# Kernel optimization log

Measured on AMD Instinct MI355X. Metric: run time of the kernel, lower is better.

The kernel has to match this reference:

```python
import jax, jax.numpy as jnp
import numpy as np
from jax.ops import segment_sum, segment_max

N_NODES, SEQ, D, V = 2048, 64, 256, 32000
NH, DH = 8, 32      # transformer heads, head dim
GH = 4              # GAT heads (concat=False -> mean over heads)
E = 32768
NEG_INF = -1e9


def _pe(max_len, d):
    pos = np.arange(max_len)[:, None].astype(np.float32)
    div = np.exp(np.arange(0, d, 2).astype(np.float32) * (-np.log(10000.0) / d))
    pe = np.zeros((max_len, d), np.float32)
    pe[:, 0::2] = np.sin(pos * div)
    pe[:, 1::2] = np.cos(pos * div)
    return jnp.asarray(pe)


def _ln(x, g, b, eps=1e-5):
    m = x.mean(-1, keepdims=True)
    v = jnp.var(x, axis=-1, keepdims=True)
    return (x - m) / jnp.sqrt(v + eps) * g + b


def _encoder(x, Wqkv, bqkv, Wo, bo, ln1g, ln1b, ln2g, ln2b, W1, b1, W2, b2):
    # nn.TransformerEncoder, post-norm, relu, dropout off (eval)
    for l in range(2):
        qkv = x @ Wqkv[l] + bqkv[l]
        q, k, v = jnp.split(qkv, 3, -1)
        hds = lambda t: t.reshape(N_NODES, SEQ, NH, DH).transpose(0, 2, 1, 3)
        q, k, v = hds(q), hds(k), hds(v)
        att = jax.nn.softmax(jnp.einsum('bhqd,bhkd->bhqk', q, k) / np.sqrt(DH).astype(np.float32), -1)
        o = jnp.einsum('bhqk,bhkd->bhqd', att, v).transpose(0, 2, 1, 3).reshape(N_NODES, SEQ, D)
        x = _ln(x + o @ Wo[l] + bo[l], ln1g[l], ln1b[l])
        ff = jax.nn.relu(x @ W1[l] + b1[l]) @ W2[l] + b2[l]
        x = _ln(x + ff, ln2g[l], ln2b[l])
    return x


def _gat(xt, W, b, asrc, adst, src, dst, emask):
    # PyG GATConv(heads=4, concat=False): self-loops added, LeakyReLU(0.2),
    # softmax over incoming edges per destination, mean over heads, + bias.
    x = (xt @ W).reshape(N_NODES, GH, D)              # [N,GH,D]
    a_s = jnp.sum(x * asrc, -1)                        # [N,GH]
    a_d = jnp.sum(x * adst, -1)
    e = jax.nn.leaky_relu(a_s[src] + a_d[dst], 0.2)    # [E,GH]
    e = jnp.where(emask[:, None], e, NEG_INF)
    e_self = jax.nn.leaky_relu(a_s + a_d, 0.2)         # [N,GH] self loops
    m = jnp.maximum(segment_max(e, dst, num_segments=N_NODES), e_self)
    w = jnp.where(emask[:, None], jnp.exp(e - m[dst]), 0.0)
    w_self = jnp.exp(e_self - m)
    denom = segment_sum(w, dst, num_segments=N_NODES) + w_self
    num = segment_sum(w[:, :, None] * x[src], dst, num_segments=N_NODES) + w_self[:, :, None] * x
    return (num / denom[:, :, None]).mean(1) + b


def setup_inputs():
    key = jax.random.key(0)
    ks = iter(jax.random.split(key, 40))
    g = lambda shape, s=0.02: jax.random.normal(next(ks), shape, jnp.float32) * s
    return dict(
        tok_emb=g((V, D)),
        enc_Wqkv=g((2, D, 3 * D)), enc_bqkv=jnp.zeros((2, 3 * D)),
        enc_Wo=g((2, D, D)), enc_bo=jnp.zeros((2, D)),
        enc_ln1_g=jnp.ones((2, D)), enc_ln1_b=jnp.zeros((2, D)),
        enc_ln2_g=jnp.ones((2, D)), enc_ln2_b=jnp.zeros((2, D)),
        enc_W1=g((2, D, D)), enc_b1=jnp.zeros((2, D)),
        enc_W2=g((2, D, D)), enc_b2=jnp.zeros((2, D)),
        type_emb=g((10, D)),
        msg_W=g((3, D, D)), msg_b=jnp.zeros((3, D)),
        gat_W=g((4, D, GH * D)), gat_b=jnp.zeros((4, D)),
        gat_asrc=g((4, GH, D)), gat_adst=g((4, GH, D)),
        sp_W1=g((D, 512)), sp_b1=jnp.zeros((512,)),
        sp_W2=g((512, D)), sp_b2=jnp.zeros((D,)),
        log_c=jnp.zeros((1,)),
        rule_token_seqs=jax.random.randint(next(ks), (N_NODES, SEQ), 0, V),
        rule_types=jax.random.randint(next(ks), (N_NODES,), 0, 10),
        edge_index=jax.random.randint(next(ks), (2, E), 0, N_NODES),
        edge_type=jax.random.randint(next(ks), (E,), 0, 3),
    )


def reference(tok_emb, enc_Wqkv, enc_bqkv, enc_Wo, enc_bo, enc_ln1_g, enc_ln1_b,
              enc_ln2_g, enc_ln2_b, enc_W1, enc_b1, enc_W2, enc_b2, type_emb,
              msg_W, msg_b, gat_W, gat_b, gat_asrc, gat_adst,
              sp_W1, sp_b1, sp_W2, sp_b2, log_c,
              rule_token_seqs, rule_types, edge_index, edge_type):
    # logic encoder
    x = tok_emb[rule_token_seqs] * np.sqrt(D).astype(np.float32) + _pe(SEQ, D)[None]
    x = _encoder(x, enc_Wqkv, enc_bqkv, enc_Wo, enc_bo, enc_ln1_g, enc_ln1_b,
                 enc_ln2_g, enc_ln2_b, enc_W1, enc_b1, enc_W2, enc_b2)
    h = x.mean(1) + type_emb[rule_types]                 # node_features [N,D]
    # logical GNN: per-relation linear + GATConv, summed, residual, relu
    src, dst = edge_index[0], edge_index[1]
    for l in range(4):
        h_new = 0.0
        for r in range(3):
            th = h @ msg_W[r] + msg_b[r]
            h_new = h_new + _gat(th, gat_W[l], gat_b[l], gat_asrc[l], gat_adst[l],
                                 src, dst, edge_type == r)
        h = jax.nn.relu(h + h_new)
    pos = jax.nn.relu(h @ sp_W1 + sp_b1) @ sp_W2 + sp_b2
    tang = jnp.tanh(pos) * 2.0
    st = tang * jnp.sqrt(jnp.exp(log_c))                 # scaled tangent [N,D]
    # Lorentz exp_map0 of v = [0, st]: ||v||_L = ||st||
    r = jnp.maximum(jnp.linalg.norm(st, axis=-1, keepdims=True), 1e-8)
    return jnp.concatenate([jnp.cosh(r), jnp.sinh(r) / r * st], -1)  # [N, D+1]
```

## Files before the change

### kernel.cpp

```cpp
#include <hip/hip_runtime.h>
#include <hip/hip_bf16.h>

#define NN 2048
#define SEQL 64
#define DIM 256
#define NHEAD 8
#define EDGES 32768
#define CROWS (NN * SEQL)
#define CHUNKS 2
#define CN (NN / CHUNKS)
#define CRC (CROWS / CHUNKS)

typedef __attribute__((ext_vector_type(8))) short short8;
typedef __attribute__((ext_vector_type(4))) float f32x4;
typedef __attribute__((ext_vector_type(4))) unsigned short us4;
typedef unsigned short ushort_t;

__device__ __forceinline__ float us2f(unsigned short u) {
    union { unsigned int i; float f; } x; x.i = ((unsigned int)u) << 16; return x.f;
}
__device__ __forceinline__ unsigned short f2us(float f) {
    union { float f; unsigned int i; } u; u.f = f;
    unsigned int r = u.i + 0x7fffu + ((u.i >> 16) & 1u);
    return (unsigned short)(r >> 16);
}
__device__ __forceinline__ float lrelu02(float v) { return v < 0.f ? 0.2f * v : v; }

__device__ __forceinline__ void gload_lds16(const void* g, void* l) {
    __builtin_amdgcn_global_load_lds(
        (const __attribute__((address_space(1))) unsigned int*)g,
        (__attribute__((address_space(3))) unsigned int*)l, 16, 0, 0);
}

__global__ void sniff_kernel(const unsigned int* __restrict__ w, int* __restrict__ flag) {
    __shared__ int cnt;
    if (threadIdx.x == 0) cnt = 0;
    __syncthreads();
    unsigned int v = w[(size_t)threadIdx.x * 509];
    unsigned int e_lo = (v >> 7) & 0xffu;
    if (e_lo >= 0x6eu && e_lo <= 0x7fu) atomicAdd(&cnt, 1);
    __syncthreads();
    if (threadIdx.x == 0) *flag = (cnt > 128) ? 1 : 0;
}

#define NE 33
struct ConvArgs {
    const void* src[NE];
    unsigned int soff[NE];
    unsigned int off[NE + 1];
    unsigned int nel[NE];
    unsigned short ncol[NE];
    unsigned char klog2[NE];
};

__global__ void convert_kernel(ConvArgs a, const int* __restrict__ flag,
                               ushort_t* __restrict__ dst, unsigned int total) {
    const int bf = *flag;
    for (unsigned int i = blockIdx.x * 256 + threadIdx.x; i < total; i += gridDim.x * 256) {
        int e = 0;
        while (a.off[e + 1] <= i) ++e;
        unsigned int j = i - a.off[e];
        ushort_t v = 0;
        if (j < a.nel[e]) {
            unsigned int sidx;
            if (a.klog2[e]) {
                unsigned int K = 1u << a.klog2[e];
                unsigned int k = j & (K - 1), n = j >> a.klog2[e];
                sidx = k * (unsigned int)a.ncol[e] + n;
            } else sidx = j;
            sidx += a.soff[e];
            if (bf) v = ((const ushort_t*)a.src[e])[sidx];
            else    v = f2us(((const float*)a.src[e])[sidx]);
        }
        dst[i] = v;
    }
}

template <int K, bool RELU, bool OUT_BF16>
__global__ __launch_bounds__(256) void gemm_bt(
    const ushort_t* __restrict__ A, const ushort_t* __restrict__ BT,
    const ushort_t* __restrict__ bias, void* __restrict__ C,
    int N, int lda, size_t a_off_z, size_t c_off_z)
{
    __shared__ __align__(16) short smem[16384];

    const int tid  = threadIdx.x;
    const int lane = tid & 63;
    const int wave = tid >> 6;
    const int wr = wave >> 1, wc = wave & 1;

    const int gx = gridDim.x, gy = gridDim.y;
    const int nwg = gx * gy;
    const int lin = blockIdx.y * gx + blockIdx.x;
    const int q8 = nwg >> 3;
    const int sid = (lin & 7) * q8 + (lin >> 3);
    const int mb = sid / gy;
    const int nb = sid - mb * gy;
    const size_t mbase = (size_t)mb * 128;
    const size_t nbase = (size_t)nb * 128;

    A += (size_t)blockIdx.z * a_off_z;
    const size_t czoff = (size_t)blockIdx.z * c_off_z;

    f32x4 acc[4][4];
    const f32x4 fzero = {0.f, 0.f, 0.f, 0.f};
#pragma unroll
    for (int i = 0; i < 4; ++i)
#pragma unroll
        for (int j = 0; j < 4; ++j) acc[i][j] = fzero;

    const int srow = tid >> 2;
    const int ksw0 = (((tid & 3) ^ ((srow >> 1) & 3)) * 8);
    const int rl = lane & 15;
    const int kfs = (((lane >> 4) ^ ((rl >> 1) & 3)) * 8);

    constexpr int nk = K >> 5;
    auto stage = [&](int buf, int k0) {
        short* lA = smem + buf * 4096 + wave * 512;
        short* lB = smem + 8192 + buf * 4096 + wave * 512;
        gload_lds16(A  + (mbase + srow)      * (size_t)lda + k0 + ksw0, lA);
        gload_lds16(A  + (mbase + srow + 64) * (size_t)lda + k0 + ksw0, lA + 2048);
        gload_lds16(BT + (nbase + srow)      * (size_t)K   + k0 + ksw0, lB);
        gload_lds16(BT + (nbase + srow + 64) * (size_t)K   + k0 + ksw0, lB + 2048);
    };

    stage(0, 0);
    if (nk > 1) stage(1, 32);
#pragma unroll
    for (int t = 0; t < nk; ++t) {
        const int cur = t & 1;
        if (t + 1 < nk) { asm volatile("s_waitcnt vmcnt(4)" ::: "memory"); }
        else            { asm volatile("s_waitcnt vmcnt(0)" ::: "memory"); }
        __builtin_amdgcn_s_barrier();
        __builtin_amdgcn_sched_barrier(0);

        short8 af[4], bfr[4];
#pragma unroll
        for (int m = 0; m < 4; ++m)
            af[m]  = *(const short8*)&smem[cur * 4096 + (wr * 64 + m * 16 + rl) * 32 + kfs];
#pragma unroll
        for (int n = 0; n < 4; ++n)
            bfr[n] = *(const short8*)&smem[8192 + cur * 4096 + (wc * 64 + n * 16 + rl) * 32 + kfs];
        asm volatile("s_waitcnt lgkmcnt(0)" ::: "memory");
        __builtin_amdgcn_sched_barrier(0);
#pragma unroll
        for (int m = 0; m < 4; ++m)
#pragma unroll
            for (int n = 0; n < 4; ++n)
                acc[m][n] = __builtin_amdgcn_mfma_f32_16x16x32_bf16(af[m], bfr[n], acc[m][n], 0, 0, 0);
        __builtin_amdgcn_s_barrier();
        __builtin_amdgcn_sched_barrier(0);
        if (t + 2 < nk) stage(cur, (t + 2) * 32);
    }

    const int rq = (lane >> 4) * 4;
    if (OUT_BF16) {
#pragma unroll
        for (int m = 0; m < 4; ++m)
#pragma unroll
            for (int n = 0; n < 4; ++n) {
                int lcol = wc * 64 + n * 16 + rl;
                float bv = bias ? us2f(bias[nbase + lcol]) : 0.f;
                int chunk = lcol >> 3;
#pragma unroll
                for (int q = 0; q < 4; ++q) {
                    int row = wr * 64 + m * 16 + rq + q;
                    float v = acc[m][n][q] + bv;
                    if (RELU) v = fmaxf(v, 0.f);
                    smem[row * 128 + (((chunk ^ (row & 7)) << 3) | (lcol & 7))] = (short)f2us(v);
                }
            }
        asm volatile("s_waitcnt lgkmcnt(0)" ::: "memory");
        __builtin_amdgcn_s_barrier();
        __builtin_amdgcn_sched_barrier(0);
#pragma unroll
        for (int j = 0; j < 8; ++j) {
            int hw = tid * 8 + j * 2048;
            int row = hw >> 7;
            int ch  = tid & 15;
            short8 v = *(const short8*)&smem[row * 128 + ((ch ^ (row & 7)) << 3)];
            *(short8*)((ushort_t*)C + czoff + (mbase + row) * (size_t)N + nbase + ch * 8) = v;
        }
    } else {
#pragma unroll
        for (int m = 0; m < 4; ++m)
#pragma unroll
            for (int n = 0; n < 4; ++n) {
                size_t gcol = nbase + wc * 64 + n * 16 + rl;
                float bv = bias ? us2f(bias[gcol]) : 0.f;
#pragma unroll
                for (int q = 0; q < 4; ++q) {
                    size_t grow = mbase + wr * 64 + m * 16 + rq + q;
                    float v = acc[m][n][q] + bv;
                    if (RELU) v = fmaxf(v, 0.f);
                    ((float*)C)[czoff + grow * N + gcol] = v;
                }
            }
    }
}

template <int K>
__global__ __launch_bounds__(512) void gemm_ln(
    const ushort_t* __restrict__ A, int lda, const ushort_t* __restrict__ BT,
    const ushort_t* __restrict__ bias, ushort_t* __restrict__ X,
    const ushort_t* __restrict__ gg, const ushort_t* __restrict__ bb)
{
    __shared__ __align__(16) short a_lds[2][128][32];
    __shared__ __align__(16) short b_lds[2][256][32];
    __shared__ float st_part[128][8];
    __shared__ float st_fin[128][2];

    const int tid  = threadIdx.x;
    const int lane = tid & 63;
    const int wave = tid >> 6;
    const int wr = wave >> 2, wc = wave & 3;
    const size_t mbase = (size_t)blockIdx.x * 128;

    f32x4 acc[4][4];
    const f32x4 fzero = {0.f, 0.f, 0.f, 0.f};
#pragma unroll
    for (int i = 0; i < 4; ++i)
#pragma unroll
        for (int j = 0; j < 4; ++j) acc[i][j] = fzero;

    const int srow = tid >> 2;
    const int ksw0 = (((tid & 3) ^ ((srow >> 1) & 3)) * 8);
    const int rl = lane & 15;
    const int g  = lane >> 4;
    const int kfs = ((g ^ ((rl >> 1) & 3)) * 8);

    constexpr int nk = K >> 5;
    auto stage = [&](int buf, int k0) {
        gload_lds16(A  + (mbase + srow) * (size_t)lda + k0 + ksw0,
                    &a_lds[buf][0][0] + wave * 512);
        gload_lds16(BT + (size_t)srow         * K + k0 + ksw0,
                    &b_lds[buf][0][0] + wave * 512);
        gload_lds16(BT + (size_t)(srow + 128) * K + k0 + ksw0,
                    &b_lds[buf][0][0] + wave * 512 + 4096);
    };

    stage(0, 0);
    if (nk > 1) stage(1, 32);
#pragma unroll
    for (int t = 0; t < nk; ++t) {
        const int cur = t & 1;
        if (t + 1 < nk) { asm volatile("s_waitcnt vmcnt(3)" ::: "memory"); }
        else            { asm volatile("s_waitcnt vmcnt(0)" ::: "memory"); }
        __builtin_amdgcn_s_barrier();
        __builtin_amdgcn_sched_barrier(0);

        short8 af[4], bfr[4];
#pragma unroll
        for (int m = 0; m < 4; ++m) af[m]  = *(const short8*)&a_lds[cur][wr * 64 + m * 16 + rl][kfs];
#pragma unroll
        for (int n = 0; n < 4; ++n) bfr[n] = *(const short8*)&b_lds[cur][wc * 64 + n * 16 + rl][kfs];
        asm volatile("s_waitcnt lgkmcnt(0)" ::: "memory");
        __builtin_amdgcn_sched_barrier(0);
#pragma unroll
        for (int m = 0; m < 4; ++m)
#pragma unroll
            for (int n = 0; n < 4; ++n)
                acc[m][n] = __builtin_amdgcn_mfma_f32_16x16x32_bf16(af[m], bfr[n], acc[m][n], 0, 0, 0);
        __builtin_amdgcn_s_barrier();
        __builtin_amdgcn_sched_barrier(0);
        if (t + 2 < nk) stage(cur, (t + 2) * 32);
    }

#pragma unroll
    for (int m = 0; m < 4; ++m)
#pragma unroll
        for (int n = 0; n < 4; ++n) {
            int gcol = wc * 64 + n * 16 + rl;
            float bv = us2f(bias[gcol]);
#pragma unroll
            for (int r = 0; r < 4; ++r) {
                size_t grow = mbase + wr * 64 + m * 16 + g * 4 + r;
                acc[m][n][r] += bv + us2f(X[grow * 256 + gcol]);
            }
        }
#pragma unroll
    for (int m = 0; m < 4; ++m)
#pragma unroll
        for (int r = 0; r < 4; ++r) {
            float ps = 0.f, pq = 0.f;
#pragma unroll
            for (int n = 0; n < 4; ++n) { float v = acc[m][n][r]; ps += v; pq += v * v; }
#pragma unroll
            for (int off = 1; off < 16; off <<= 1) { ps += __shfl_xor(ps, off); pq += __shfl_xor(pq, off); }
            if (rl == 0) {
                int row = wr * 64 + m * 16 + g * 4 + r;
                st_part[row][wc] = ps;
                st_part[row][4 + wc] = pq;
            }
        }
    __syncthreads();
    if (tid < 128) {
        float s = st_part[tid][0] + st_part[tid][1] + st_part[tid][2] + st_part[tid][3];
        float q = st_part[tid][4] + st_part[tid][5] + st_part[tid][6] + st_part[tid][7];
        float mean = s * (1.f / 256.f);
        float var = q * (1.f / 256.f) - mean * mean;
        st_fin[tid][0] = mean;
        st_fin[tid][1] = rsqrtf(var + 1e-5f);
    }
    __syncthreads();
#pragma unroll
    for (int m = 0; m < 4; ++m)
#pragma unroll
        for (int n = 0; n < 4; ++n) {
            int gcol = wc * 64 + n * 16 + rl;
            float gv = us2f(gg[gcol]), bv = us2f(bb[gcol]);
#pragma unroll
            for (int r = 0; r < 4; ++r) {
                int row = wr * 64 + m * 16 + g * 4 + r;
                float out = (acc[m][n][r] - st_fin[row][0]) * st_fin[row][1] * gv + bv;
                X[(mbase + row) * 256 + gcol] = f2us(out);
            }
        }
}

__global__ __launch_bounds__(256) void ffn_ln(
    ushort_t* __restrict__ X,
    const ushort_t* __restrict__ W1T, const ushort_t* __restrict__ b1,
    const ushort_t* __restrict__ W2T, const ushort_t* __restrict__ b2,
    const ushort_t* __restrict__ gg, const ushort_t* __restrict__ bb)
{
    __shared__ __align__(16) short a_lds[2][64][32];
    __shared__ __align__(16) short b_lds[2][256][32];
    __shared__ __align__(16) short T[64 * 256];
    __shared__ float st_part[64][8];
    __shared__ float st_fin[64][2];

    const int tid  = threadIdx.x;
    const int lane = tid & 63;
    const int wc   = tid >> 6;
    const size_t mbase = (size_t)blockIdx.x * 64;
    const int rl = lane & 15;
    const int g  = lane >> 4;
    const int kfs = ((g ^ ((rl >> 1) & 3)) * 8);

    const int arow = tid >> 2;
    const int ksw0 = (((tid & 3) ^ ((arow >> 1) & 3)) * 8);

    f32x4 acc[4][4];
    const f32x4 fzero = {0.f, 0.f, 0.f, 0.f};
#pragma unroll
    for (int i = 0; i < 4; ++i)
#pragma unroll
        for (int j = 0; j < 4; ++j) acc[i][j] = fzero;

    auto stage1 = [&](int buf, int k0) {
        gload_lds16(X + (mbase + arow) * (size_t)256 + k0 + ksw0,
                    &a_lds[buf][0][0] + wc * 512);
#pragma unroll
        for (int p = 0; p < 4; ++p)
            gload_lds16(W1T + (size_t)(arow + p * 64) * 256 + k0 + ksw0,
                        &b_lds[buf][0][0] + p * 2048 + wc * 512);
    };
    auto stage2 = [&](int buf, int k0) {
#pragma unroll
        for (int p = 0; p < 4; ++p)
            gload_lds16(W2T + (size_t)(arow + p * 64) * 256 + k0 + ksw0,
                        &b_lds[buf][0][0] + p * 2048 + wc * 512);
    };

    stage1(0, 0);
    stage1(1, 32);
#pragma unroll
    for (int t = 0; t < 8; ++t) {
        const int cur = t & 1;
        if (t + 1 < 8) { asm volatile("s_waitcnt vmcnt(5)" ::: "memory"); }
        else           { asm volatile("s_waitcnt vmcnt(0)" ::: "memory"); }
        __builtin_amdgcn_s_barrier();
        __builtin_amdgcn_sched_barrier(0);

        short8 af[4], bfr[4];
#pragma unroll
        for (int m = 0; m < 4; ++m) af[m]  = *(const short8*)&a_lds[cur][m * 16 + rl][kfs];
#pragma unroll
        for (int n = 0; n < 4; ++n) bfr[n] = *(const short8*)&b_lds[cur][wc * 64 + n * 16 + rl][kfs];
        asm volatile("s_waitcnt lgkmcnt(0)" ::: "memory");
        __builtin_amdgcn_sched_barrier(0);
#pragma unroll
        for (int m = 0; m < 4; ++m)
#pragma unroll
            for (int n = 0; n < 4; ++n)
                acc[m][n] = __builtin_amdgcn_mfma_f32_16x16x32_bf16(af[m], bfr[n], acc[m][n], 0, 0, 0);
        __builtin_amdgcn_s_barrier();
        __builtin_amdgcn_sched_barrier(0);
        if (t + 2 < 8) stage1(cur, (t + 2) * 32);
    }

    stage2(0, 0);
    stage2(1, 32);

#pragma unroll
    for (int m = 0; m < 4; ++m)
#pragma unroll
        for (int n = 0; n < 4; ++n) {
            int lcol = wc * 64 + n * 16 + rl;
            float bv = us2f(b1[lcol]);
            int chunk = lcol >> 3;
#pragma unroll
            for (int q = 0; q < 4; ++q) {
                int row = m * 16 + g * 4 + q;
                float v = fmaxf(acc[m][n][q] + bv, 0.f);
                T[row * 256 + (((chunk ^ (row & 7)) << 3) | (lcol & 7))] = (short)f2us(v);
            }
            acc[m][n] = fzero;
        }
    asm volatile("s_waitcnt lgkmcnt(0)" ::: "memory");
    __builtin_amdgcn_s_barrier();
    __builtin_amdgcn_sched_barrier(0);

#pragma unroll
    for (int t = 0; t < 8; ++t) {
        const int cur = t & 1;
        if (t + 1 < 8) { asm volatile("s_waitcnt vmcnt(4)" ::: "memory"); }
        else           { asm volatile("s_waitcnt vmcnt(0)" ::: "memory"); }
        __builtin_amdgcn_s_barrier();
        __builtin_amdgcn_sched_barrier(0);

        short8 af[4], bfr[4];
#pragma unroll
        for (int m = 0; m < 4; ++m) {
            int row = m * 16 + rl;
            af[m] = *(const short8*)&T[row * 256 + (((t * 4 + g) ^ (row & 7)) << 3)];
        }
#pragma unroll
        for (int n = 0; n < 4; ++n) bfr[n] = *(const short8*)&b_lds[cur][wc * 64 + n * 16 + rl][kfs];
        asm volatile("s_waitcnt lgkmcnt(0)" ::: "memory");
        __builtin_amdgcn_sched_barrier(0);
#pragma unroll
        for (int m = 0; m < 4; ++m)
#pragma unroll
            for (int n = 0; n < 4; ++n)
                acc[m][n] = __builtin_amdgcn_mfma_f32_16x16x32_bf16(af[m], bfr[n], acc[m][n], 0, 0, 0);
        __builtin_amdgcn_s_barrier();
        __builtin_amdgcn_sched_barrier(0);
        if (t + 2 < 8) stage2(cur, (t + 2) * 32);
    }

#pragma unroll
    for (int m = 0; m < 4; ++m)
#pragma unroll
        for (int n = 0; n < 4; ++n) {
            int gcol = wc * 64 + n * 16 + rl;
            float bv = us2f(b2[gcol]);
#pragma unroll
            for (int r = 0; r < 4; ++r) {
                size_t grow = mbase + m * 16 + g * 4 + r;
                acc[m][n][r] += bv + us2f(X[grow * 256 + gcol]);
            }
        }
#pragma unroll
    for (int m = 0; m < 4; ++m)
#pragma unroll
        for (int r = 0; r < 4; ++r) {
            float ps = 0.f, pq = 0.f;
#pragma unroll
            for (int n = 0; n < 4; ++n) { float v = acc[m][n][r]; ps += v; pq += v * v; }
#pragma unroll
            for (int off = 1; off < 16; off <<= 1) { ps += __shfl_xor(ps, off); pq += __shfl_xor(pq, off); }
            if (rl == 0) {
                int row = m * 16 + g * 4 + r;
                st_part[row][wc] = ps;
                st_part[row][4 + wc] = pq;
            }
        }
    __syncthreads();
    if (tid < 64) {
        float s = st_part[tid][0] + st_part[tid][1] + st_part[tid][2] + st_part[tid][3];
        float q = st_part[tid][4] + st_part[tid][5] + st_part[tid][6] + st_part[tid][7];
        float mean = s * (1.f / 256.f);
        float var = q * (1.f / 256.f) - mean * mean;
        st_fin[tid][0] = mean;
        st_fin[tid][1] = rsqrtf(var + 1e-5f);
    }
    __syncthreads();
#pragma unroll
    for (int m = 0; m < 4; ++m)
#pragma unroll
        for (int n = 0; n < 4; ++n) {
            int gcol = wc * 64 + n * 16 + rl;
            float gv = us2f(gg[gcol]), bv = us2f(bb[gcol]);
#pragma unroll
            for (int r = 0; r < 4; ++r) {
                int row = m * 16 + g * 4 + r;
                float out = (acc[m][n][r] - st_fin[row][0]) * st_fin[row][1] * gv + bv;
                X[(mbase + row) * 256 + gcol] = f2us(out);
            }
        }
}

__global__ __launch_bounds__(128) void attn_mfma(ushort_t* __restrict__ qkv) {
    __shared__ ushort_t smem[2][6912];
    const int w = threadIdx.x >> 6, lane = threadIdx.x & 63;
    const int h = blockIdx.y * 2 + w;
    const int rl = lane & 15, g = lane >> 4;
    const size_t rowbase = (size_t)blockIdx.x * 64;
    ushort_t* vt = smem[w];
    ushort_t* pl = smem[w] + 2304;

    const ushort_t* vp = qkv + (rowbase + lane) * 768 + 512 + h * 32;
#pragma unroll
    for (int i = 0; i < 4; ++i) {
        union { short8 v; ushort_t s[8]; } u;
        u.v = *(const short8*)(vp + i * 8);
#pragma unroll
        for (int j = 0; j < 8; ++j) vt[(i * 8 + j) * 72 + lane] = u.s[j];
    }

    short8 kf[4], qf[4];
#pragma unroll
    for (int t = 0; t < 4; ++t) {
        kf[t] = *(const short8*)(qkv + (rowbase + t * 16 + rl) * 768 + 256 + h * 32 + g * 8);
        qf[t] = *(const short8*)(qkv + (rowbase + t * 16 + rl) * 768 +       h * 32 + g * 8);
    }

    f32x4 s[4][4];
    const f32x4 fzero = {0.f, 0.f, 0.f, 0.f};
#pragma unroll
    for (int kt = 0; kt < 4; ++kt)
#pragma unroll
        for (int qt = 0; qt < 4; ++qt) s[kt][qt] = fzero;
#pragma unroll
    for (int kt = 0; kt < 4; ++kt)
#pragma unroll
        for (int qt = 0; qt < 4; ++qt)
            s[kt][qt] = __builtin_amdgcn_mfma_f32_16x16x32_bf16(kf[kt], qf[qt], s[kt][qt], 0, 0, 0);

    const float sc = 0.17677669529663687f;
    float inv[4];
#pragma unroll
    for (int qt = 0; qt < 4; ++qt) {
        float m = -1e30f;
#pragma unroll
        for (int kt = 0; kt < 4; ++kt)
#pragma unroll
            for (int r = 0; r < 4; ++r) { s[kt][qt][r] *= sc; m = fmaxf(m, s[kt][qt][r]); }
        m = fmaxf(m, __shfl_xor(m, 16));
        m = fmaxf(m, __shfl_xor(m, 32));
        float sum = 0.f;
#pragma unroll
        for (int kt = 0; kt < 4; ++kt)
#pragma unroll
            for (int r = 0; r < 4; ++r) { float e = __expf(s[kt][qt][r] - m); s[kt][qt][r] = e; sum += e; }
        sum += __shfl_xor(sum, 16);
        sum += __shfl_xor(sum, 32);
        inv[qt] = 1.f / sum;
    }

#pragma unroll
    for (int qt = 0; qt < 4; ++qt)
#pragma unroll
        for (int kt = 0; kt < 4; ++kt) {
            us4 pk;
#pragma unroll
            for (int r = 0; r < 4; ++r) pk[r] = f2us(s[kt][qt][r] * inv[qt]);
            *(us4*)&pl[(qt * 16 + rl) * 72 + kt * 16 + g * 4] = pk;
        }
    asm volatile("s_waitcnt lgkmcnt(0)" ::: "memory");
    __builtin_amdgcn_sched_barrier(0);

    f32x4 o[2][4];
#pragma unroll
    for (int dt = 0; dt < 2; ++dt)
#pragma unroll
        for (int qt = 0; qt < 4; ++qt) o[dt][qt] = fzero;
#pragma unroll
    for (int ks = 0; ks < 2; ++ks) {
        short8 va[2];
#pragma unroll
        for (int dt = 0; dt < 2; ++dt)
            va[dt] = *(const short8*)&vt[(dt * 16 + rl) * 72 + ks * 32 + g * 8];
#pragma unroll
        for (int qt = 0; qt < 4; ++qt) {
            short8 pb = *(const short8*)&pl[(qt * 16 + rl) * 72 + ks * 32 + g * 8];
#pragma unroll
            for (int dt = 0; dt < 2; ++dt)
                o[dt][qt] = __builtin_amdgcn_mfma_f32_16x16x32_bf16(va[dt], pb, o[dt][qt], 0, 0, 0);
        }
    }

#pragma unroll
    for (int dt = 0; dt < 2; ++dt)
#pragma unroll
        for (int qt = 0; qt < 4; ++qt) {
            us4 ov;
#pragma unroll
            for (int r = 0; r < 4; ++r) ov[r] = f2us(o[dt][qt][r]);
            *(us4*)&pl[(qt * 16 + rl) * 40 + dt * 16 + g * 4] = ov;
        }
    asm volatile("s_waitcnt lgkmcnt(0)" ::: "memory");
    __builtin_amdgcn_sched_barrier(0);
    ushort_t* op = qkv + (rowbase + lane) * 768 + h * 32;
#pragma unroll
    for (int t = 0; t < 4; ++t)
        *(short8*)(op + t * 8) = *(const short8*)&pl[lane * 40 + t * 8];
}

__global__ void pe_kernel(float* __restrict__ pe) {
    int s = blockIdx.x, d = threadIdx.x;
    int i = d >> 1;
    float freq = __expf((float)(2 * i) * (-9.210340371976184f / 256.f));
    float ang = (float)s * freq;
    pe[s * DIM + d] = (d & 1) ? cosf(ang) : sinf(ang);
}

__global__ __launch_bounds__(256) void embed_kernel(const void* __restrict__ tok_emb,
                                                    const int* __restrict__ flag,
                                                    const int* __restrict__ tokens,
                                                    const float* __restrict__ pe,
                                                    ushort_t* __restrict__ X) {
    int grow = blockIdx.x * 4 + (threadIdx.x >> 6);
    int t = threadIdx.x & 63;
    int tok = tokens[grow];
    int s = grow & 63;
    int d0 = t * 4;
    size_t idx = (size_t)tok * DIM + d0;
    f32x4 pv = *(const f32x4*)&pe[s * DIM + d0];
    us4 out;
    if (*flag) {
        us4 tv = *(const us4*)((const ushort_t*)tok_emb + idx);
#pragma unroll
        for (int j = 0; j < 4; ++j) out[j] = f2us(us2f(tv[j]) * 16.f + pv[j]);
    } else {
        f32x4 tv = *(const f32x4*)((const float*)tok_emb + idx);
#pragma unroll
        for (int j = 0; j < 4; ++j) out[j] = f2us(tv[j] * 16.f + pv[j]);
    }
    *(us4*)&X[(size_t)grow * DIM + d0] = out;
}

__global__ void mean_kernel(const ushort_t* __restrict__ Xc,
                            const ushort_t* __restrict__ type_emb,
                            const int* __restrict__ rtypes,
                            float* __restrict__ h, ushort_t* __restrict__ hb) {
    int n = blockIdx.x, d = threadIdx.x;
    float acc = 0.f;
    for (int s = 0; s < 64; ++s) acc += us2f(Xc[((size_t)n * 64 + s) * DIM + d]);
    float val = acc * (1.f / 64.f) + us2f(type_emb[(size_t)rtypes[n] * DIM + d]);
    h[(size_t)n * DIM + d] = val;
    hb[(size_t)n * DIM + d] = f2us(val);
}

__global__ void hist_kernel(const int* __restrict__ ei, int* __restrict__ counts) {
    int e = blockIdx.x * 256 + threadIdx.x;
    if (e < EDGES) atomicAdd(&counts[ei[EDGES + e]], 1);
}
__global__ __launch_bounds__(256) void scan_kernel(const int* __restrict__ counts,
                                                   int* __restrict__ indptr,
                                                   int* __restrict__ cursor) {
    __shared__ int part[256];
    int t = threadIdx.x;
    int local[8]; int s = 0;
#pragma unroll
    for (int i = 0; i < 8; ++i) { local[i] = s; s += counts[t * 8 + i]; }
    part[t] = s;
    __syncthreads();
    for (int d = 1; d < 256; d <<= 1) {
        int val = (t >= d) ? part[t - d] : 0;
        __syncthreads();
        part[t] += val;
        __syncthreads();
    }
    int base = part[t] - s;
#pragma unroll
    for (int i = 0; i < 8; ++i) { int v = base + local[i]; indptr[t * 8 + i] = v; cursor[t * 8 + i] = v; }
    if (t == 255) indptr[NN] = part[255];
}
__global__ void scatter_kernel(const int* __restrict__ ei, const int* __restrict__ et,
                               int* __restrict__ cursor, int* __restrict__ col_src,
                               int* __restrict__ col_type) {
    int e = blockIdx.x * 256 + threadIdx.x;
    if (e < EDGES) {
        int d = ei[EDGES + e];
        int pp = atomicAdd(&cursor[d], 1);
        col_src[pp] = ei[e];
        col_type[pp] = et[e];
    }
}

__global__ __launch_bounds__(256) void asad_kernel(const ushort_t* __restrict__ xg,
                                                   const ushort_t* __restrict__ asrc,
                                                   const ushort_t* __restrict__ adst,
                                                   float* __restrict__ a_s, float* __restrict__ a_d,
                                                   int l) {
    int n = blockIdx.x, r = blockIdx.y, g = threadIdx.x >> 6, lane = threadIdx.x & 63;
    const ushort_t* xp = xg + ((size_t)r * NN + n) * 1024 + g * 256 + lane * 4;
    const ushort_t* sp = asrc + ((size_t)l * 4 + g) * 256 + lane * 4;
    const ushort_t* dp = adst + ((size_t)l * 4 + g) * 256 + lane * 4;
    us4 xv = *(const us4*)xp;
    float ss = 0.f, dd = 0.f;
#pragma unroll
    for (int j = 0; j < 4; ++j) { float x = us2f(xv[j]); ss += x * us2f(sp[j]); dd += x * us2f(dp[j]); }
#pragma unroll
    for (int off = 32; off > 0; off >>= 1) { ss += __shfl_xor(ss, off); dd += __shfl_xor(dd, off); }
    if (lane == 0) {
        a_s[((size_t)r * NN + n) * 4 + g] = ss;
        a_d[((size_t)r * NN + n) * 4 + g] = dd;
    }
}

__global__ __launch_bounds__(256) void edge_kernel(const ushort_t* __restrict__ xg,
                                                   const float* __restrict__ a_s,
                                                   const float* __restrict__ a_d,
                                                   const int* __restrict__ indptr,
                                                   const int* __restrict__ col_src,
                                                   const int* __restrict__ col_type,
                                                   const ushort_t* __restrict__ gat_b,
                                                   float* __restrict__ hnew3, int l) {
    __shared__ float outs[4][256];
    int n = blockIdx.x, r = blockIdx.y, g = threadIdx.x >> 6, lane = threadIdx.x & 63;
    int beg = indptr[n], end = indptr[n + 1];
    const size_t rb = (size_t)r * NN;
    float adn = a_d[(rb + n) * 4 + g];
    float eself = lrelu02(a_s[(rb + n) * 4 + g] + adn);
    float m = eself;
    for (int e = beg; e < end; ++e) {
        if (col_type[e] == r) {
            float v = lrelu02(a_s[(rb + col_src[e]) * 4 + g] + adn);
            m = fmaxf(m, v);
        }
    }
    float wself = __expf(eself - m);
    float denom = wself;
    us4 xn = *(const us4*)(xg + (rb + n) * 1024 + g * 256 + lane * 4);
    float num[4];
#pragma unroll
    for (int j = 0; j < 4; ++j) num[j] = wself * us2f(xn[j]);
    for (int e = beg; e < end; ++e) {
        if (col_type[e] == r) {
            int src = col_src[e];
            float v = lrelu02(a_s[(rb + src) * 4 + g] + adn);
            float w = __expf(v - m);
            denom += w;
            us4 xs = *(const us4*)(xg + (rb + src) * 1024 + g * 256 + lane * 4);
#pragma unroll
            for (int j = 0; j < 4; ++j) num[j] += w * us2f(xs[j]);
        }
    }
    float invd = 1.f / denom;
#pragma unroll
    for (int j = 0; j < 4; ++j) outs[g][lane * 4 + j] = num[j] * invd;
    __syncthreads();
    int d = threadIdx.x;
    float hv = 0.25f * (outs[0][d] + outs[1][d] + outs[2][d] + outs[3][d]) + us2f(gat_b[l * 256 + d]);
    hnew3[(rb + n) * 256 + d] = hv;
}

__global__ void update_h_kernel(float* __restrict__ h, const float* __restrict__ hnew3,
                                ushort_t* __restrict__ hb) {
    size_t i = (size_t)blockIdx.x * 256 + threadIdx.x;
    float v = fmaxf(h[i] + hnew3[i] + hnew3[(size_t)NN * 256 + i] + hnew3[(size_t)2 * NN * 256 + i], 0.f);
    h[i] = v;
    hb[i] = f2us(v);
}

__global__ __launch_bounds__(64) void final_kernel(const float* __restrict__ pos,
                                                   const ushort_t* __restrict__ log_c,
                                                   const int* __restrict__ flag,
                                                   void* __restrict__ out) {
    int n = blockIdx.x, lane = threadIdx.x;
    int bf = *flag;
    float scv = sqrtf(__expf(us2f(log_c[0])));
    f32x4 pv = *(const f32x4*)&pos[(size_t)n * 256 + lane * 4];
    float st[4]; float sq = 0.f;
#pragma unroll
    for (int j = 0; j < 4; ++j) { float t = tanhf(pv[j]) * 2.f * scv; st[j] = t; sq += t * t; }
#pragma unroll
    for (int off = 32; off > 0; off >>= 1) sq += __shfl_xor(sq, off);
    float rr = fmaxf(sqrtf(sq), 1e-8f);
    float sf = sinhf(rr) / rr;
    if (bf) {
        ushort_t* o = (ushort_t*)out;
        if (lane == 0) o[(size_t)n * 257] = f2us(coshf(rr));
#pragma unroll
        for (int j = 0; j < 4; ++j) o[(size_t)n * 257 + 1 + lane * 4 + j] = f2us(sf * st[j]);
    } else {
        float* o = (float*)out;
        if (lane == 0) o[(size_t)n * 257] = coshf(rr);
#pragma unroll
        for (int j = 0; j < 4; ++j) o[(size_t)n * 257 + 1 + lane * 4 + j] = sf * st[j];
    }
}

extern "C" void kernel_launch(void* const* d_in, const int* in_sizes, int n_in,
                              void* d_out, int out_size, void* d_ws, size_t ws_size,
                              hipStream_t stream) {
    const int* tokens = (const int*)d_in[25];
    const int* rtypes = (const int*)d_in[26];
    const int* eidx   = (const int*)d_in[27];
    const int* etype  = (const int*)d_in[28];

    char* base = (char*)d_ws;
    size_t pos = 0;
    auto alloc = [&](size_t b) -> char* {
        char* r = base + pos; pos = (pos + b + 255) & ~(size_t)255; return r;
    };

    int* flag = (int*)alloc(256);

    ConvArgs ca;
    int ne = 0; unsigned int off = 0;
    auto add = [&](const void* src, unsigned int soff, unsigned int elems,
                   int klog2, int ncol) -> unsigned int {
        ca.src[ne] = src; ca.soff[ne] = soff; ca.off[ne] = off;
        ca.nel[ne] = elems; ca.klog2[ne] = (unsigned char)klog2;
        ca.ncol[ne] = (unsigned short)ncol;
        unsigned int r = off; off += (elems + 7) & ~7u; ++ne; return r;
    };
    unsigned int oWqkv = add(d_in[1], 0, 196608, 8, 768);
                         add(d_in[1], 196608, 196608, 8, 768);
    unsigned int obqkv = add(d_in[2], 0, 1536, 0, 0);
    unsigned int oWo   = add(d_in[3], 0, 65536, 8, 256);
                         add(d_in[3], 65536, 65536, 8, 256);
    unsigned int obo   = add(d_in[4], 0, 512, 0, 0);
    unsigned int oln1g = add(d_in[5], 0, 512, 0, 0);
    unsigned int oln1b = add(d_in[6], 0, 512, 0, 0);
    unsigned int oln2g = add(d_in[7], 0, 512, 0, 0);
    unsigned int oln2b = add(d_in[8], 0, 512, 0, 0);
    unsigned int oW1   = add(d_in[9], 0, 65536, 8, 256);
                         add(d_in[9], 65536, 65536, 8, 256);
    unsigned int ob1   = add(d_in[10], 0, 512, 0, 0);
    unsigned int oW2   = add(d_in[11], 0, 65536, 8, 256);
                         add(d_in[11], 65536, 65536, 8, 256);
    unsigned int ob2   = add(d_in[12], 0, 512, 0, 0);
    unsigned int otype = add(d_in[13], 0, 2560, 0, 0);
    unsigned int omsgW = add(d_in[14], 0, 65536, 8, 256);
                         add(d_in[14], 65536, 65536, 8, 256);
                         add(d_in[14], 131072, 65536, 8, 256);
    unsigned int omsgb = add(d_in[15], 0, 768, 0, 0);
    unsigned int ogatW = add(d_in[16], 0, 262144, 8, 1024);
                         add(d_in[16], 262144, 262144, 8, 1024);
                         add(d_in[16], 524288, 262144, 8, 1024);
                         add(d_in[16], 786432, 262144, 8, 1024);
    unsigned int ogatb = add(d_in[17], 0, 1024, 0, 0);
    unsigned int oasrc = add(d_in[18], 0, 4096, 0, 0);
    unsigned int oadst = add(d_in[19], 0, 4096, 0, 0);
    unsigned int ospW1 = add(d_in[20], 0, 131072, 8, 512);
    unsigned int ospb1 = add(d_in[21], 0, 512, 0, 0);
    unsigned int ospW2 = add(d_in[22], 0, 131072, 9, 256);
    unsigned int ospb2 = add(d_in[23], 0, 256, 0, 0);
    unsigned int ologc = add(d_in[24], 0, 1, 0, 0);
    ca.off[ne] = off;
    unsigned int wtotal = off;

    ushort_t* wtb   = (ushort_t*)alloc((size_t)wtotal * 2);
    float*    pe    = (float*)   alloc((size_t)SEQL * DIM * 4);
    float*    h     = (float*)   alloc((size_t)NN * DIM * 4);
    ushort_t* hb    = (ushort_t*)alloc((size_t)NN * DIM * 2);
    float*    a_s   = (float*)   alloc((size_t)3 * NN * 4 * 4);
    float*    a_d   = (float*)   alloc((size_t)3 * NN * 4 * 4);
    int*      counts = (int*)    alloc((size_t)NN * 4);
    int*      indptr = (int*)    alloc((size_t)(NN + 1) * 4);
    int*      cursor = (int*)    alloc((size_t)NN * 4);
    int*      col_src  = (int*)  alloc((size_t)EDGES * 4);
    int*      col_type = (int*)  alloc((size_t)EDGES * 4);

    ushort_t* Xc  = (ushort_t*)alloc((size_t)CROWS * DIM * 2);
    size_t spos0 = pos;
    ushort_t* QKV = (ushort_t*)alloc((size_t)CRC * 768 * 2);
    pos = spos0;
    ushort_t* th    = (ushort_t*)alloc((size_t)NN * 768 * 2);
    ushort_t* xg    = (ushort_t*)alloc((size_t)3 * NN * 1024 * 2);
    float*    hnew3 = (float*)   alloc((size_t)3 * NN * DIM * 4);
    ushort_t* thead = (ushort_t*)alloc((size_t)NN * 512 * 2);
    float*    posb  = (float*)   alloc((size_t)NN * DIM * 4);

    const ushort_t* WqkvT = wtb + oWqkv;
    const ushort_t* bqkv  = wtb + obqkv;
    const ushort_t* WoT   = wtb + oWo;
    const ushort_t* bo    = wtb + obo;
    const ushort_t* ln1g  = wtb + oln1g;
    const ushort_t* ln1b  = wtb + oln1b;
    const ushort_t* ln2g  = wtb + oln2g;
    const ushort_t* ln2b  = wtb + oln2b;
    const ushort_t* W1T   = wtb + oW1;
    const ushort_t* b1    = wtb + ob1;
    const ushort_t* W2T   = wtb + oW2;
    const ushort_t* b2    = wtb + ob2;
    const ushort_t* type_emb = wtb + otype;
    const ushort_t* msgWT = wtb + omsgW;
    const ushort_t* msg_b = wtb + omsgb;
    const ushort_t* gatWT = wtb + ogatW;
    const ushort_t* gat_b = wtb + ogatb;
    const ushort_t* gasrc = wtb + oasrc;
    const ushort_t* gadst = wtb + oadst;
    const ushort_t* spW1T = wtb + ospW1;
    const ushort_t* spb1  = wtb + ospb1;
    const ushort_t* spW2T = wtb + ospW2;
    const ushort_t* spb2  = wtb + ospb2;
    const ushort_t* log_c = wtb + ologc;

    sniff_kernel<<<1, 256, 0, stream>>>((const unsigned int*)d_in[1], flag);
    convert_kernel<<<2048, 256, 0, stream>>>(ca, flag, wtb, wtotal);

    pe_kernel<<<SEQL, DIM, 0, stream>>>(pe);
    hipMemsetAsync(counts, 0, NN * 4, stream);
    hist_kernel<<<EDGES / 256, 256, 0, stream>>>(eidx, counts);
    scan_kernel<<<1, 256, 0, stream>>>(counts, indptr, cursor);
    scatter_kernel<<<EDGES / 256, 256, 0, stream>>>(eidx, etype, cursor, col_src, col_type);

    embed_kernel<<<CROWS / 4, 256, 0, stream>>>(d_in[0], flag, tokens, pe, Xc);
    for (int c = 0; c < CHUNKS; ++c) {
        ushort_t* Xcc = Xc + (size_t)c * CRC * DIM;
        for (int l = 0; l < 2; ++l) {
            gemm_bt<256, false, true><<<dim3(CRC / 128, 6), 256, 0, stream>>>(
                Xcc, WqkvT + (size_t)l * 196608, bqkv + l * 768, QKV, 768, DIM, 0, 0);
            attn_mfma<<<dim3(CN, 4), 128, 0, stream>>>(QKV);
            gemm_ln<256><<<CRC / 128, 512, 0, stream>>>(
                QKV, 768, WoT + (size_t)l * 65536, bo + l * DIM, Xcc, ln1g + l * DIM, ln1b + l * DIM);
            ffn_ln<<<CRC / 64, 256, 0, stream>>>(
                Xcc, W1T + (size_t)l * 65536, b1 + l * DIM, W2T + (size_t)l * 65536, b2 + l * DIM,
                ln2g + l * DIM, ln2b + l * DIM);
        }
    }
    mean_kernel<<<NN, DIM, 0, stream>>>(Xc, type_emb, rtypes, h, hb);

    for (int l = 0; l < 4; ++l) {
        gemm_bt<256, false, true><<<dim3(NN / 128, 6), 256, 0, stream>>>(
            hb, msgWT, msg_b, th, 768, DIM, 0, 0);
        gemm_bt<256, false, true><<<dim3(NN / 128, 8, 3), 256, 0, stream>>>(
            th, gatWT + (size_t)l * 262144, nullptr, xg, 1024, 768,
            (size_t)256, (size_t)NN * 1024);
        asad_kernel<<<dim3(NN, 3), 256, 0, stream>>>(xg, gasrc, gadst, a_s, a_d, l);
        edge_kernel<<<dim3(NN, 3), 256, 0, stream>>>(xg, a_s, a_d, indptr, col_src, col_type,
                                                     gat_b, hnew3, l);
        update_h_kernel<<<NN, 256, 0, stream>>>(h, hnew3, hb);
    }

    gemm_bt<256, true, true><<<dim3(NN / 128, 4), 256, 0, stream>>>(
        hb, spW1T, spb1, thead, 512, DIM, 0, 0);
    gemm_bt<512, false, false><<<dim3(NN / 128, 2), 256, 0, stream>>>(
        thead, spW2T, spb2, posb, DIM, 512, 0, 0);
    final_kernel<<<NN, 64, 0, stream>>>(posb, log_c, flag, d_out);
}
```

Measured before the change: 1.133 ms.

## Load GEMM operands directly from global memory into MFMA registers, dropping LDS staging

```diff
diff --git a/kernel.cpp b/kernel.cpp
--- a/kernel.cpp
+++ b/kernel.cpp
@@ -199,14 +199,115 @@
     }
 }
 
+template <int K, bool RELU, bool OUT_BF16>
+__global__ __launch_bounds__(256) void gemm_direct(
+    const ushort_t* __restrict__ A, const ushort_t* __restrict__ BT,
+    const ushort_t* __restrict__ bias, void* __restrict__ C,
+    int N, int lda, size_t a_off_z, size_t c_off_z)
+{
+    __shared__ __align__(16) short smem[16384];
+
+    const int tid  = threadIdx.x;
+    const int lane = tid & 63;
+    const int wave = tid >> 6;
+    const int wr = wave >> 1, wc = wave & 1;
+
+    const int gx = gridDim.x, gy = gridDim.y;
+    const int nwg = gx * gy;
+    const int lin = blockIdx.y * gx + blockIdx.x;
+    const int q8 = nwg >> 3;
+    const int sid = (lin & 7) * q8 + (lin >> 3);
+    const int mb = sid / gy;
+    const int nb = sid - mb * gy;
+    const size_t mbase = (size_t)mb * 128;
+    const size_t nbase = (size_t)nb * 128;
+
+    A += (size_t)blockIdx.z * a_off_z;
+    const size_t czoff = (size_t)blockIdx.z * c_off_z;
+
+    const int rl = lane & 15;
+    const int kf = (lane >> 4) * 8;
+
+    f32x4 acc[4][4];
+    const f32x4 fzero = {0.f, 0.f, 0.f, 0.f};
+#pragma unroll
+    for (int i = 0; i < 4; ++i)
+#pragma unroll
+        for (int j = 0; j < 4; ++j) acc[i][j] = fzero;
+
+    const ushort_t* ap[4];
+    const ushort_t* bp[4];
+#pragma unroll
+    for (int m = 0; m < 4; ++m) ap[m] = A  + (mbase + wr * 64 + m * 16 + rl) * (size_t)lda + kf;
+#pragma unroll
+    for (int n = 0; n < 4; ++n) bp[n] = BT + (nbase + wc * 64 + n * 16 + rl) * (size_t)K   + kf;
+
+#pragma unroll
+    for (int t = 0; t < (K >> 5); ++t) {
+        short8 af[4], bfr[4];
+#pragma unroll
+        for (int m = 0; m < 4; ++m) af[m]  = *(const short8*)(ap[m] + t * 32);
+#pragma unroll
+        for (int n = 0; n < 4; ++n) bfr[n] = *(const short8*)(bp[n] + t * 32);
+#pragma unroll
+        for (int m = 0; m < 4; ++m)
+#pragma unroll
+            for (int n = 0; n < 4; ++n)
+                acc[m][n] = __builtin_amdgcn_mfma_f32_16x16x32_bf16(af[m], bfr[n], acc[m][n], 0, 0, 0);
+    }
+
+    const int rq = (lane >> 4) * 4;
+    if (OUT_BF16) {
+#pragma unroll
+        for (int m = 0; m < 4; ++m)
+#pragma unroll
+            for (int n = 0; n < 4; ++n) {
+                int lcol = wc * 64 + n * 16 + rl;
+                float bv = bias ? us2f(bias[nbase + lcol]) : 0.f;
+                int chunk = lcol >> 3;
+#pragma unroll
+                for (int q = 0; q < 4; ++q) {
+                    int row = wr * 64 + m * 16 + rq + q;
+                    float v = acc[m][n][q] + bv;
+                    if (RELU) v = fmaxf(v, 0.f);
+                    smem[row * 128 + (((chunk ^ (row & 7)) << 3) | (lcol & 7))] = (short)f2us(v);
+                }
+            }
+        asm volatile("s_waitcnt lgkmcnt(0)" ::: "memory");
+        __builtin_amdgcn_s_barrier();
+        __builtin_amdgcn_sched_barrier(0);
+#pragma unroll
+        for (int j = 0; j < 8; ++j) {
+            int hw = tid * 8 + j * 2048;
+            int row = hw >> 7;
+            int ch  = tid & 15;
+            short8 v = *(const short8*)&smem[row * 128 + ((ch ^ (row & 7)) << 3)];
+            *(short8*)((ushort_t*)C + czoff + (mbase + row) * (size_t)N + nbase + ch * 8) = v;
+        }
+    } else {
+#pragma unroll
+        for (int m = 0; m < 4; ++m)
+#pragma unroll
+            for (int n = 0; n < 4; ++n) {
+                size_t gcol = nbase + wc * 64 + n * 16 + rl;
+                float bv = bias ? us2f(bias[gcol]) : 0.f;
+#pragma unroll
+                for (int q = 0; q < 4; ++q) {
+                    size_t grow = mbase + wr * 64 + m * 16 + rq + q;
+                    float v = acc[m][n][q] + bv;
+                    if (RELU) v = fmaxf(v, 0.f);
+                    ((float*)C)[czoff + grow * N + gcol] = v;
+                }
+            }
+    }
+}
+
 template <int K>
 __global__ __launch_bounds__(512) void gemm_ln(
     const ushort_t* __restrict__ A, int lda, const ushort_t* __restrict__ BT,
     const ushort_t* __restrict__ bias, ushort_t* __restrict__ X,
     const ushort_t* __restrict__ gg, const ushort_t* __restrict__ bb)
 {
-    __shared__ __align__(16) short a_lds[2][128][32];
-    __shared__ __align__(16) short b_lds[2][256][32];
     __shared__ float st_part[128][8];
     __shared__ float st_fin[128][2];
 
@@ -215,6 +316,9 @@
     const int wave = tid >> 6;
     const int wr = wave >> 2, wc = wave & 3;
     const size_t mbase = (size_t)blockIdx.x * 128;
+    const int rl = lane & 15;
+    const int g  = lane >> 4;
+    const int kf = g * 8;
 
     f32x4 acc[4][4];
     const f32x4 fzero = {0.f, 0.f, 0.f, 0.f};
@@ -223,47 +327,25 @@
 #pragma unroll
         for (int j = 0; j < 4; ++j) acc[i][j] = fzero;
 
-    const int srow = tid >> 2;
-    const int ksw0 = (((tid & 3) ^ ((srow >> 1) & 3)) * 8);
-    const int rl = lane & 15;
-    const int g  = lane >> 4;
-    const int kfs = ((g ^ ((rl >> 1) & 3)) * 8);
-
-    constexpr int nk = K >> 5;
-    auto stage = [&](int buf, int k0) {
-        gload_lds16(A  + (mbase + srow) * (size_t)lda + k0 + ksw0,
-                    &a_lds[buf][0][0] + wave * 512);
-        gload_lds16(BT + (size_t)srow         * K + k0 + ksw0,
-                    &b_lds[buf][0][0] + wave * 512);
-        gload_lds16(BT + (size_t)(srow + 128) * K + k0 + ksw0,
-                    &b_lds[buf][0][0] + wave * 512 + 4096);
-    };
-
-    stage(0, 0);
-    if (nk > 1) stage(1, 32);
-#pragma unroll
-    for (int t = 0; t < nk; ++t) {
-        const int cur = t & 1;
-        if (t + 1 < nk) { asm volatile("s_waitcnt vmcnt(3)" ::: "memory"); }
-        else            { asm volatile("s_waitcnt vmcnt(0)" ::: "memory"); }
-        __builtin_amdgcn_s_barrier();
-        __builtin_amdgcn_sched_barrier(0);
-
+    const ushort_t* ap[4];
+    const ushort_t* bp[4];
+#pragma unroll
+    for (int m = 0; m < 4; ++m) ap[m] = A  + (mbase + wr * 64 + m * 16 + rl) * (size_t)lda + kf;
+#pragma unroll
+    for (int n = 0; n < 4; ++n) bp[n] = BT + (size_t)(wc * 64 + n * 16 + rl) * K + kf;
+
+#pragma unroll
+    for (int t = 0; t < (K >> 5); ++t) {
         short8 af[4], bfr[4];
 #pragma unroll
-        for (int m = 0; m < 4; ++m) af[m]  = *(const short8*)&a_lds[cur][wr * 64 + m * 16 + rl][kfs];
-#pragma unroll
-        for (int n = 0; n < 4; ++n) bfr[n] = *(const short8*)&b_lds[cur][wc * 64 + n * 16 + rl][kfs];
-        asm volatile("s_waitcnt lgkmcnt(0)" ::: "memory");
-        __builtin_amdgcn_sched_barrier(0);
+        for (int m = 0; m < 4; ++m) af[m]  = *(const short8*)(ap[m] + t * 32);
+#pragma unroll
+        for (int n = 0; n < 4; ++n) bfr[n] = *(const short8*)(bp[n] + t * 32);
 #pragma unroll
         for (int m = 0; m < 4; ++m)
 #pragma unroll
             for (int n = 0; n < 4; ++n)
                 acc[m][n] = __builtin_amdgcn_mfma_f32_16x16x32_bf16(af[m], bfr[n], acc[m][n], 0, 0, 0);
-        __builtin_amdgcn_s_barrier();
-        __builtin_amdgcn_sched_barrier(0);
-        if (t + 2 < nk) stage(cur, (t + 2) * 32);
     }
 
 #pragma unroll
@@ -324,8 +406,6 @@
     const ushort_t* __restrict__ W2T, const ushort_t* __restrict__ b2,
     const ushort_t* __restrict__ gg, const ushort_t* __restrict__ bb)
 {
-    __shared__ __align__(16) short a_lds[2][64][32];
-    __shared__ __align__(16) short b_lds[2][256][32];
     __shared__ __align__(16) short T[64 * 256];
     __shared__ float st_part[64][8];
     __shared__ float st_fin[64][2];
@@ -336,10 +416,7 @@
     const size_t mbase = (size_t)blockIdx.x * 64;
     const int rl = lane & 15;
     const int g  = lane >> 4;
-    const int kfs = ((g ^ ((rl >> 1) & 3)) * 8);
-
-    const int arow = tid >> 2;
-    const int ksw0 = (((tid & 3) ^ ((arow >> 1) & 3)) * 8);
+    const int kf = g * 8;
 
     f32x4 acc[4][4];
     const f32x4 fzero = {0.f, 0.f, 0.f, 0.f};
@@ -348,50 +425,26 @@
 #pragma unroll
         for (int j = 0; j < 4; ++j) acc[i][j] = fzero;
 
-    auto stage1 = [&](int buf, int k0) {
-        gload_lds16(X + (mbase + arow) * (size_t)256 + k0 + ksw0,
-                    &a_lds[buf][0][0] + wc * 512);
-#pragma unroll
-        for (int p = 0; p < 4; ++p)
-            gload_lds16(W1T + (size_t)(arow + p * 64) * 256 + k0 + ksw0,
-                        &b_lds[buf][0][0] + p * 2048 + wc * 512);
-    };
-    auto stage2 = [&](int buf, int k0) {
-#pragma unroll
-        for (int p = 0; p < 4; ++p)
-            gload_lds16(W2T + (size_t)(arow + p * 64) * 256 + k0 + ksw0,
-                        &b_lds[buf][0][0] + p * 2048 + wc * 512);
-    };
-
-    stage1(0, 0);
-    stage1(1, 32);
+    const ushort_t* ap[4];
+    const ushort_t* bp[4];
+#pragma unroll
+    for (int m = 0; m < 4; ++m) ap[m] = X   + (mbase + m * 16 + rl) * (size_t)256 + kf;
+#pragma unroll
+    for (int n = 0; n < 4; ++n) bp[n] = W1T + (size_t)(wc * 64 + n * 16 + rl) * 256 + kf;
+
 #pragma unroll
     for (int t = 0; t < 8; ++t) {
-        const int cur = t & 1;
-        if (t + 1 < 8) { asm volatile("s_waitcnt vmcnt(5)" ::: "memory"); }
-        else           { asm volatile("s_waitcnt vmcnt(0)" ::: "memory"); }
-        __builtin_amdgcn_s_barrier();
-        __builtin_amdgcn_sched_barrier(0);
-
         short8 af[4], bfr[4];
 #pragma unroll
-        for (int m = 0; m < 4; ++m) af[m]  = *(const short8*)&a_lds[cur][m * 16 + rl][kfs];
-#pragma unroll
-        for (int n = 0; n < 4; ++n) bfr[n] = *(const short8*)&b_lds[cur][wc * 64 + n * 16 + rl][kfs];
-        asm volatile("s_waitcnt lgkmcnt(0)" ::: "memory");
-        __builtin_amdgcn_sched_barrier(0);
+        for (int m = 0; m < 4; ++m) af[m]  = *(const short8*)(ap[m] + t * 32);
+#pragma unroll
+        for (int n = 0; n < 4; ++n) bfr[n] = *(const short8*)(bp[n] + t * 32);
 #pragma unroll
         for (int m = 0; m < 4; ++m)
 #pragma unroll
             for (int n = 0; n < 4; ++n)
                 acc[m][n] = __builtin_amdgcn_mfma_f32_16x16x32_bf16(af[m], bfr[n], acc[m][n], 0, 0, 0);
-        __builtin_amdgcn_s_barrier();
-        __builtin_amdgcn_sched_barrier(0);
-        if (t + 2 < 8) stage1(cur, (t + 2) * 32);
-    }
-
-    stage2(0, 0);
-    stage2(1, 32);
+    }
 
 #pragma unroll
     for (int m = 0; m < 4; ++m)
@@ -408,18 +461,12 @@
             }
             acc[m][n] = fzero;
         }
-    asm volatile("s_waitcnt lgkmcnt(0)" ::: "memory");
-    __builtin_amdgcn_s_barrier();
-    __builtin_amdgcn_sched_barrier(0);
-
+    __syncthreads();
+
+#pragma unroll
+    for (int n = 0; n < 4; ++n) bp[n] = W2T + (size_t)(wc * 64 + n * 16 + rl) * 256 + kf;
 #pragma unroll
     for (int t = 0; t < 8; ++t) {
-        const int cur = t & 1;
-        if (t + 1 < 8) { asm volatile("s_waitcnt vmcnt(4)" ::: "memory"); }
-        else           { asm volatile("s_waitcnt vmcnt(0)" ::: "memory"); }
-        __builtin_amdgcn_s_barrier();
-        __builtin_amdgcn_sched_barrier(0);
-
         short8 af[4], bfr[4];
 #pragma unroll
         for (int m = 0; m < 4; ++m) {
@@ -427,17 +474,12 @@
             af[m] = *(const short8*)&T[row * 256 + (((t * 4 + g) ^ (row & 7)) << 3)];
         }
 #pragma unroll
-        for (int n = 0; n < 4; ++n) bfr[n] = *(const short8*)&b_lds[cur][wc * 64 + n * 16 + rl][kfs];
-        asm volatile("s_waitcnt lgkmcnt(0)" ::: "memory");
-        __builtin_amdgcn_sched_barrier(0);
+        for (int n = 0; n < 4; ++n) bfr[n] = *(const short8*)(bp[n] + t * 32);
 #pragma unroll
         for (int m = 0; m < 4; ++m)
 #pragma unroll
             for (int n = 0; n < 4; ++n)
                 acc[m][n] = __builtin_amdgcn_mfma_f32_16x16x32_bf16(af[m], bfr[n], acc[m][n], 0, 0, 0);
-        __builtin_amdgcn_s_barrier();
-        __builtin_amdgcn_sched_barrier(0);
-        if (t + 2 < 8) stage2(cur, (t + 2) * 32);
     }
 
 #pragma unroll
@@ -919,9 +961,9 @@
     mean_kernel<<<NN, DIM, 0, stream>>>(Xc, type_emb, rtypes, h, hb);
 
     for (int l = 0; l < 4; ++l) {
-        gemm_bt<256, false, true><<<dim3(NN / 128, 6), 256, 0, stream>>>(
+        gemm_direct<256, false, true><<<dim3(NN / 128, 6), 256, 0, stream>>>(
             hb, msgWT, msg_b, th, 768, DIM, 0, 0);
-        gemm_bt<256, false, true><<<dim3(NN / 128, 8, 3), 256, 0, stream>>>(
+        gemm_direct<256, false, true><<<dim3(NN / 128, 8, 3), 256, 0, stream>>>(
             th, gatWT + (size_t)l * 262144, nullptr, xg, 1024, 768,
             (size_t)256, (size_t)NN * 1024);
         asad_kernel<<<dim3(NN, 3), 256, 0, stream>>>(xg, gasrc, gadst, a_s, a_d, l);
@@ -930,9 +972,9 @@
         update_h_kernel<<<NN, 256, 0, stream>>>(h, hnew3, hb);
     }
 
-    gemm_bt<256, true, true><<<dim3(NN / 128, 4), 256, 0, stream>>>(
+    gemm_direct<256, true, true><<<dim3(NN / 128, 4), 256, 0, stream>>>(
         hb, spW1T, spb1, thead, 512, DIM, 0, 0);
-    gemm_bt<512, false, false><<<dim3(NN / 128, 2), 256, 0, stream>>>(
+    gemm_direct<512, false, false><<<dim3(NN / 128, 2), 256, 0, stream>>>(
         thead, spW2T, spb2, posb, DIM, 512, 0, 0);
     final_kernel<<<NN, 64, 0, stream>>>(posb, log_c, flag, d_out);
 }
```

New measurement: 1.316 ms. 16.2% more time.
